# Kernel tuning notes

Hardware: AMD Instinct MI355X
Metric: run time of the kernel (lower is better)

The kernel has to match this reference:

```python
import jax, jax.numpy as jnp
import numpy as np
from jax import lax

B, L, F = 32, 2048, 76   # batch, seq_len, feat_dim
H = 128                  # conv hidden channels
D = 128                  # prototype dim (last 1x1 conv)
P = 128                  # number of prototypes
CLASS_SIZE = 2


def setup_inputs() -> dict:
    key = jax.random.key(0)
    ks = jax.random.split(key, 8)
    w = lambda k, shape: jax.random.normal(k, shape, jnp.float32) * 0.05
    return {
        "x": jax.random.normal(ks[0], (B, L, F), jnp.float32),
        "W1": w(ks[1], (H, F, 5)), "b1": jnp.zeros((H,), jnp.float32),
        "W2": w(ks[2], (H, H, 5)), "b2": jnp.zeros((H,), jnp.float32),
        "W3": w(ks[3], (H, H, 5)), "b3": jnp.zeros((H,), jnp.float32),
        "Wo1": w(ks[4], (D, H)), "bo1": jnp.zeros((D,), jnp.float32),
        "Wo2": w(ks[5], (D, D)), "bo2": jnp.zeros((D,), jnp.float32),
        "prototypes": jax.random.uniform(ks[6], (P, D), jnp.float32),
        "protop_classes": jnp.concatenate([jnp.zeros(P // 2, jnp.int32), jnp.ones(P // 2, jnp.int32)]),
    }


def _conv1d_same(h, W, b):
    # h: (B, C, L), W: (O, C, K=5), symmetric padding 2 == torch padding=k//2
    y = lax.conv_general_dilated(h, W, window_strides=(1,), padding=[(2, 2)],
                                 dimension_numbers=("NCW", "OIW", "NCW"))
    return y + b[None, :, None]


def _maxpool2(h):
    return lax.reduce_window(h, -jnp.inf, lax.max, (1, 1, 2), (1, 1, 2), "VALID")


def reference(x, W1, b1, W2, b2, W3, b3, Wo1, bo1, Wo2, bo2, prototypes, protop_classes):
    h = jnp.transpose(x, (0, 2, 1))  # (B, F, L)
    for W, b in ((W1, b1), (W2, b2), (W3, b3)):
        h = _maxpool2(jax.nn.relu(_conv1d_same(h, W, b)))
    # 1x1 convs as channel matmuls
    h = jax.nn.relu(jnp.einsum("bcl,oc->bol", h, Wo1) + bo1[None, :, None])
    h = jax.nn.relu(jnp.einsum("bcl,oc->bol", h, Wo2) + bo2[None, :, None])
    f = jnp.transpose(h, (0, 2, 1))  # (B, Lp=256, D)
    # l2_conv via ||a-b||^2 = ||a||^2 - 2 a.b + ||b||^2 (same math, GEMM form)
    d2 = (jnp.sum(f * f, axis=-1, keepdims=True)
          - 2.0 * jnp.einsum("bld,pd->blp", f, prototypes)
          + jnp.sum(prototypes * prototypes, axis=-1))  # (B, Lp, P)
    dis = jnp.sqrt(jnp.maximum(d2, 1e-12))
    min_dis = jnp.min(dis, axis=1)  # (B, P): min over patches
    # dis2sim, 'log' activation
    sim = jnp.log((min_dis + 1.0) / (min_dis + 1e-4))
    # init_weights: last_layer.weight[i,j] = 1 if protop_classes[j]==i else -0.5
    lw = jnp.where(protop_classes[None, :] == jnp.arange(CLASS_SIZE)[:, None], 1.0, -0.5)
    out = jax.nn.sigmoid(sim @ lw.T)  # (B, CLASS_SIZE)
    return out, min_dis
```

## Files before the change

kernel.cpp:

```cpp
#include <hip/hip_runtime.h>
#include <cmath>


typedef __attribute__((ext_vector_type(8))) short short8;
typedef __attribute__((ext_vector_type(4))) float f32x4;

__device__ __forceinline__ unsigned short f2bf(float v) {
    union { float f; unsigned u; } x; x.f = v;
    unsigned r = x.u + 0x7fffu + ((x.u >> 16) & 1u);
    return (unsigned short)(r >> 16);
}
__device__ __forceinline__ float bf2f(unsigned short b) {
    union { unsigned u; float f; } x; x.u = ((unsigned)b) << 16;
    return x.f;
}

__device__ void pack_conv_w(int t, int total, const float* __restrict__ W, int C,
                            unsigned short* __restrict__ dst)
{
    if (t >= total) return;
    int lane = t & 63, rest = t >> 6;
    int mf = rest & 7; rest >>= 3;
    int kk = rest % 5, cc = rest / 5;
    int m = mf * 16 + (lane & 15);
    int cb = cc * 32 + (lane >> 4) * 8;
    unsigned short v[8];
#pragma unroll
    for (int j = 0; j < 8; ++j) {
        int c = cb + j;
        v[j] = (c < C) ? f2bf(W[((size_t)m * C + c) * 5 + kk]) : (unsigned short)0;
    }
    *(uint4*)&dst[(size_t)t * 8] = *(uint4*)v;
}

__device__ void pack_mat(int t, const float* __restrict__ M, unsigned short* __restrict__ dst)
{
    if (t >= 2048) return;
    int lane = t & 63, mf = (t >> 6) & 7, cc = t >> 9;
    int m = mf * 16 + (lane & 15);
    int c0 = cc * 32 + (lane >> 4) * 8;
    unsigned short v[8];
#pragma unroll
    for (int j = 0; j < 8; ++j) v[j] = f2bf(M[(size_t)m * 128 + c0 + j]);
    *(uint4*)&dst[(size_t)t * 8] = *(uint4*)v;
}

__global__ __launch_bounds__(256)
void prep_weights_kernel(const float* __restrict__ W1, const float* __restrict__ W2,
                         const float* __restrict__ W3, const float* __restrict__ Wo1,
                         const float* __restrict__ Wo2, const float* __restrict__ protos,
                         unsigned short* A1, unsigned short* A2, unsigned short* A3,
                         unsigned short* AW1, unsigned short* AW2, unsigned short* AP,
                         float* pn, unsigned* pm_bits)
{
    int t = blockIdx.x * 256 + threadIdx.x;
    switch (blockIdx.y) {
    case 0: pack_conv_w(t, 7680,  W1, 76,  A1); break;
    case 1: pack_conv_w(t, 10240, W2, 128, A2); break;
    case 2: pack_conv_w(t, 10240, W3, 128, A3); break;
    case 3: pack_mat(t, Wo1, AW1); break;
    case 4: pack_mat(t, Wo2, AW2); break;
    case 5: pack_mat(t, protos, AP); break;
    case 6:
        if (t < 128) {
            float s = 0.f;
            for (int d = 0; d < 128; ++d) {
                float v = bf2f(f2bf(protos[(size_t)t * 128 + d]));
                s = fmaf(v, v, s);
            }
            pn[t] = s;
        }
        break;
    case 7:
        if (t < 4096) pm_bits[t] = 0x7F800000u;
        break;
    }
}

template <int NJ, int NCC, int STRIDE, int ROWOFF, int ROWMAX>
__device__ __forceinline__ void conv_k(const unsigned short* __restrict__ Af,
                                       const unsigned short* __restrict__ sIn,
                                       int nbase, int mf0, int lane,
                                       f32x4 (&acc)[2][NJ])
{
    const int lc = lane & 15;
    const int lk = (lane >> 4) * 8;
#pragma unroll
    for (int i = 0; i < 2; ++i)
#pragma unroll
        for (int j = 0; j < NJ; ++j) acc[i][j] = (f32x4){0.f, 0.f, 0.f, 0.f};

    for (int cc = 0; cc < NCC; ++cc) {
#pragma unroll
        for (int kk = 0; kk < 5; ++kk) {
            const int step = cc * 5 + kk;
            short8 a[2];
#pragma unroll
            for (int i = 0; i < 2; ++i)
                a[i] = *(const short8*)&Af[(((size_t)step * 8 + mf0 + i) * 64 + lane) * 8];
            short8 bb[NJ];
#pragma unroll
            for (int j = 0; j < NJ; ++j) {
                int row = nbase + j * 16 + lc + kk + ROWOFF;
                if (ROWMAX >= 0) row = min(max(row, 0), ROWMAX);
                bb[j] = *(const short8*)&sIn[row * STRIDE + cc * 32 + lk];
            }
#pragma unroll
            for (int j = 0; j < NJ; ++j)
#pragma unroll
                for (int i = 0; i < 2; ++i)
                    acc[i][j] = __builtin_amdgcn_mfma_f32_16x16x32_bf16(a[i], bb[j], acc[i][j], 0, 0, 0);
        }
    }
}

__device__ __forceinline__ void gemm_head(const unsigned short* __restrict__ Af,
                                          const unsigned short* __restrict__ s_f,
                                          int nbase, int mf0, int lane,
                                          f32x4 (&acc)[2])
{
    const int lc = lane & 15;
    const int lk = (lane >> 4) * 8;
    acc[0] = (f32x4){0.f, 0.f, 0.f, 0.f};
    acc[1] = (f32x4){0.f, 0.f, 0.f, 0.f};
#pragma unroll
    for (int cc = 0; cc < 4; ++cc) {
        short8 a[2];
#pragma unroll
        for (int i = 0; i < 2; ++i)
            a[i] = *(const short8*)&Af[(((size_t)cc * 8 + mf0 + i) * 64 + lane) * 8];
        short8 bb = *(const short8*)&s_f[(nbase + lc) * 136 + cc * 32 + lk];
#pragma unroll
        for (int i = 0; i < 2; ++i)
            acc[i] = __builtin_amdgcn_mfma_f32_16x16x32_bf16(a[i], bb, acc[i], 0, 0, 0);
    }
}

__global__ __launch_bounds__(512, 2)
void mega_kernel(const float* __restrict__ x,
                 const unsigned short* __restrict__ A1, const float* __restrict__ b1,
                 const unsigned short* __restrict__ A2, const float* __restrict__ b2,
                 const unsigned short* __restrict__ A3, const float* __restrict__ b3,
                 const unsigned short* __restrict__ AW1, const float* __restrict__ bo1,
                 const unsigned short* __restrict__ AW2, const float* __restrict__ bo2,
                 const unsigned short* __restrict__ AP,  const float* __restrict__ pn,
                 unsigned* __restrict__ pm_bits)
{
    __shared__ __align__(16) unsigned short s_x[324 * 104];
    __shared__ __align__(16) unsigned short s_h1[140 * 136];
    __shared__ float s_cb[768];
    __shared__ float s_part[128];
    __shared__ float s_fn[32];
    unsigned short* s_h2 = s_x;
    unsigned short* s_f  = s_x + 9248;

    const int tid  = threadIdx.x;
    const int q    = blockIdx.x;
    const int b    = blockIdx.y;
    const int lane = tid & 63;
    const int wid  = tid >> 6;
    const int mf0  = (wid & 3) * 2;
    const int ng   = wid >> 2;
    const int lc   = lane & 15;
    const int lq   = (lane >> 4) * 4;

    for (int i = tid; i < 768; i += 512) {
        const float* src = (i < 128) ? b1 : (i < 256) ? b2 : (i < 384) ? b3
                         : (i < 512) ? bo1 : (i < 640) ? bo2 : pn;
        s_cb[i] = src[i & 127];
    }

    const int xbase = 256 * q - 18;
    for (int idx = tid; idx < 324 * 24; idx += 512) {
        int pos = idx / 24, c0 = (idx % 24) * 4;
        int l = xbase + pos;
        unsigned short v[4] = {0, 0, 0, 0};
        if (c0 < 76 && l >= 0 && l < 2048) {
            float4 xv = *(const float4*)&x[((size_t)b * 2048 + l) * 76 + c0];
            v[0] = f2bf(xv.x); v[1] = f2bf(xv.y); v[2] = f2bf(xv.z); v[3] = f2bf(xv.w);
        }
        *(uint2*)&s_x[pos * 104 + c0] = *(uint2*)v;
    }
    __syncthreads();

    {
        f32x4 acc[2][10];
        conv_k<10, 3, 104, 0, -1>(A1, s_x, ng * 160, mf0, lane, acc);

#pragma unroll
        for (int i = 0; i < 2; ++i) {
            const int ch0 = (mf0 + i) * 16 + lq;
#pragma unroll
            for (int j = 0; j < 10; ++j) {
                const int nl = ng * 160 + j * 16 + lc;
                unsigned short pk[4];
#pragma unroll
                for (int r = 0; r < 4; ++r) {
                    float v = fmaxf(acc[i][j][r] + s_cb[ch0 + r], 0.f);
                    float o = __shfl_xor(v, 1);
                    pk[r] = f2bf(fmaxf(v, o));
                }
                if ((lc & 1) == 0) {
                    int jh = (nl >> 1) - 2;
                    int jg = 128 * q - 6 + jh;
                    if (jh >= 0 && jh < 140) {
                        uint2 val = (jg >= 0 && jg < 1024) ? *(uint2*)pk : make_uint2(0u, 0u);
                        *(uint2*)&s_h1[jh * 136 + ch0] = val;
                    }
                }
            }
        }
    }
    __syncthreads();

    {
        f32x4 acc[2][6];
        conv_k<6, 4, 136, -4, 139>(A2, s_h1, ng * 96, mf0, lane, acc);

#pragma unroll
        for (int i = 0; i < 2; ++i) {
            const int ch0 = (mf0 + i) * 16 + lq;
#pragma unroll
            for (int j = 0; j < 6; ++j) {
                const int nl = ng * 96 + j * 16 + lc;
                unsigned short pk[4];
#pragma unroll
                for (int r = 0; r < 4; ++r) {
                    float v = fmaxf(acc[i][j][r] + s_cb[128 + ch0 + r], 0.f);
                    float o = __shfl_xor(v, 1);
                    pk[r] = f2bf(fmaxf(v, o));
                }
                if ((lc & 1) == 0) {
                    int jh = (nl >> 1) - 2;
                    int jg = 64 * q - 2 + jh;
                    if (jh >= 0 && jh < 68) {
                        uint2 val = (jg >= 0 && jg < 512) ? *(uint2*)pk : make_uint2(0u, 0u);
                        *(uint2*)&s_h2[jh * 136 + ch0] = val;
                    }
                }
            }
        }
    }
    __syncthreads();

    {
        f32x4 acc[2][2];
        conv_k<2, 4, 136, 0, -1>(A3, s_h2, ng * 32, mf0, lane, acc);

#pragma unroll
        for (int i = 0; i < 2; ++i) {
            const int ch0 = (mf0 + i) * 16 + lq;
#pragma unroll
            for (int j = 0; j < 2; ++j) {
                const int nl = ng * 32 + j * 16 + lc;
                unsigned short pk[4];
#pragma unroll
                for (int r = 0; r < 4; ++r) {
                    float v = fmaxf(acc[i][j][r] + s_cb[256 + ch0 + r], 0.f);
                    float o = __shfl_xor(v, 1);
                    pk[r] = f2bf(fmaxf(v, o));
                }
                if ((lc & 1) == 0)
                    *(uint2*)&s_f[(nl >> 1) * 136 + ch0] = *(uint2*)pk;
            }
        }
    }
    __syncthreads();

    f32x4 hacc[2];

    gemm_head(AW1, s_f, ng * 16, mf0, lane, hacc);
    __syncthreads();
#pragma unroll
    for (int i = 0; i < 2; ++i) {
        const int ch0 = (mf0 + i) * 16 + lq;
        unsigned short pk[4];
#pragma unroll
        for (int r = 0; r < 4; ++r)
            pk[r] = f2bf(fmaxf(hacc[i][r] + s_cb[384 + ch0 + r], 0.f));
        *(uint2*)&s_f[(ng * 16 + lc) * 136 + ch0] = *(uint2*)pk;
    }
    __syncthreads();

    gemm_head(AW2, s_f, ng * 16, mf0, lane, hacc);
    __syncthreads();
#pragma unroll
    for (int i = 0; i < 2; ++i) {
        const int ch0 = (mf0 + i) * 16 + lq;
        unsigned short pk[4];
#pragma unroll
        for (int r = 0; r < 4; ++r)
            pk[r] = f2bf(fmaxf(hacc[i][r] + s_cb[512 + ch0 + r], 0.f));
        *(uint2*)&s_f[(ng * 16 + lc) * 136 + ch0] = *(uint2*)pk;
    }
    __syncthreads();

    if (tid < 128) {
        int n = tid >> 2, part = tid & 3;
        float s = 0.f;
        for (int c = part * 32; c < part * 32 + 32; ++c) {
            float v = bf2f(s_f[n * 136 + c]);
            s = fmaf(v, v, s);
        }
        s_part[part * 32 + n] = s;
    }
    __syncthreads();
    if (tid < 32)
        s_fn[tid] = s_part[tid] + s_part[32 + tid] + s_part[64 + tid] + s_part[96 + tid];
    __syncthreads();

    gemm_head(AP, s_f, ng * 16, mf0, lane, hacc);
#pragma unroll
    for (int i = 0; i < 2; ++i) {
#pragma unroll
        for (int r = 0; r < 4; ++r) {
            const int p = (mf0 + i) * 16 + lq + r;
            const int n = ng * 16 + lc;
            float d2 = s_fn[n] + s_cb[640 + p] - 2.f * hacc[i][r];
            float m = sqrtf(fmaxf(d2, 1e-12f));
#pragma unroll
            for (int s = 1; s < 16; s <<= 1)
                m = fminf(m, __shfl_xor(m, s));
            if (lc == 0)
                atomicMin(&pm_bits[(size_t)b * 128 + p], __float_as_uint(m));
        }
    }
}

__global__ __launch_bounds__(128)
void finalize_kernel(const float* __restrict__ pm,
                     const int* __restrict__ classes,
                     float* __restrict__ out)
{
    __shared__ float r0[128], r1[128];
    const int b = blockIdx.x, p = threadIdx.x;
    float m = pm[(size_t)b * 128 + p];
    out[64 + b * 128 + p] = m;

    float sim = logf((m + 1.0f) / (m + 1e-4f));
    int cls = classes[p];
    r0[p] = (cls == 0) ? sim : -0.5f * sim;
    r1[p] = (cls == 1) ? sim : -0.5f * sim;
    __syncthreads();
    for (int s = 64; s > 0; s >>= 1) {
        if (p < s) { r0[p] += r0[p + s]; r1[p] += r1[p + s]; }
        __syncthreads();
    }
    if (p == 0) {
        out[b * 2 + 0] = 1.f / (1.f + expf(-r0[0]));
        out[b * 2 + 1] = 1.f / (1.f + expf(-r1[0]));
    }
}

extern "C" void kernel_launch(void* const* d_in, const int* in_sizes, int n_in,
                              void* d_out, int out_size, void* d_ws, size_t ws_size,
                              hipStream_t stream)
{
    (void)in_sizes; (void)n_in; (void)out_size; (void)ws_size;
    const float* x    = (const float*)d_in[0];
    const float* W1   = (const float*)d_in[1];
    const float* b1   = (const float*)d_in[2];
    const float* W2   = (const float*)d_in[3];
    const float* b2   = (const float*)d_in[4];
    const float* W3   = (const float*)d_in[5];
    const float* b3   = (const float*)d_in[6];
    const float* Wo1  = (const float*)d_in[7];
    const float* bo1  = (const float*)d_in[8];
    const float* Wo2  = (const float*)d_in[9];
    const float* bo2  = (const float*)d_in[10];
    const float* prot = (const float*)d_in[11];
    const int*   cls  = (const int*)d_in[12];
    float* out = (float*)d_out;

    char* ws = (char*)d_ws;
    unsigned short* A1  = (unsigned short*)(ws);
    unsigned short* A2  = (unsigned short*)(ws + 122880);
    unsigned short* A3  = (unsigned short*)(ws + 286720);
    unsigned short* AW1 = (unsigned short*)(ws + 450560);
    unsigned short* AW2 = (unsigned short*)(ws + 483328);
    unsigned short* AP  = (unsigned short*)(ws + 516096);
    float*          pn  = (float*)(ws + 548864);
    unsigned*       pm  = (unsigned*)(ws + 549376);

    prep_weights_kernel<<<dim3(40, 8), 256, 0, stream>>>(W1, W2, W3, Wo1, Wo2, prot,
                                                         A1, A2, A3, AW1, AW2, AP, pn, pm);
    mega_kernel<<<dim3(8, 32), 512, 0, stream>>>(x, A1, b1, A2, b2, A3, b3,
                                                 AW1, bo1, AW2, bo2, AP, pn, pm);
    finalize_kernel<<<32, 128, 0, stream>>>((const float*)pm, cls, out);
}
```

Measured before the change: 130.4 us.

## Halve sequence tile per block and widen per-wave channel tiles

Each block now covers 128 input positions instead of 256, using 256 threads and a 16x32 grid, which doubles the block count to better fill the CUs. Each wave now computes 4 channel fragments instead of 2, reusing each loaded B fragment across more MFMAs. The halo overhead per block grows relatively (196 rows loaded for 128 outputs), so there is more redundant conv work at the tile edges. Register pressure per wave also rises from the larger accumulator arrays.

Measured after the change: 130.2 us. No clear change (-0.1%).

```diff
diff --git a/kernel.cpp b/kernel.cpp
--- a/kernel.cpp
+++ b/kernel.cpp
@@ -77,16 +77,16 @@
     }
 }
 
-template <int NJ, int NCC, int STRIDE, int ROWOFF, int ROWMAX>
+template <int NJ, int NCC, int STRIDE, int ROWMAX>
 __device__ __forceinline__ void conv_k(const unsigned short* __restrict__ Af,
                                        const unsigned short* __restrict__ sIn,
                                        int nbase, int mf0, int lane,
-                                       f32x4 (&acc)[2][NJ])
+                                       f32x4 (&acc)[4][NJ])
 {
     const int lc = lane & 15;
     const int lk = (lane >> 4) * 8;
 #pragma unroll
-    for (int i = 0; i < 2; ++i)
+    for (int i = 0; i < 4; ++i)
 #pragma unroll
         for (int j = 0; j < NJ; ++j) acc[i][j] = (f32x4){0.f, 0.f, 0.f, 0.f};
 
@@ -94,21 +94,21 @@
 #pragma unroll
         for (int kk = 0; kk < 5; ++kk) {
             const int step = cc * 5 + kk;
-            short8 a[2];
-#pragma unroll
-            for (int i = 0; i < 2; ++i)
+            short8 a[4];
+#pragma unroll
+            for (int i = 0; i < 4; ++i)
                 a[i] = *(const short8*)&Af[(((size_t)step * 8 + mf0 + i) * 64 + lane) * 8];
             short8 bb[NJ];
 #pragma unroll
             for (int j = 0; j < NJ; ++j) {
-                int row = nbase + j * 16 + lc + kk + ROWOFF;
-                if (ROWMAX >= 0) row = min(max(row, 0), ROWMAX);
+                int row = nbase + j * 16 + lc + kk;
+                if (ROWMAX >= 0) row = min(row, ROWMAX);
                 bb[j] = *(const short8*)&sIn[row * STRIDE + cc * 32 + lk];
             }
 #pragma unroll
             for (int j = 0; j < NJ; ++j)
 #pragma unroll
-                for (int i = 0; i < 2; ++i)
+                for (int i = 0; i < 4; ++i)
                     acc[i][j] = __builtin_amdgcn_mfma_f32_16x16x32_bf16(a[i], bb[j], acc[i][j], 0, 0, 0);
         }
     }
@@ -116,8 +116,7 @@
 
 __device__ __forceinline__ void gemm_head(const unsigned short* __restrict__ Af,
                                           const unsigned short* __restrict__ s_f,
-                                          int nbase, int mf0, int lane,
-                                          f32x4 (&acc)[2])
+                                          int mf0h, int lane, f32x4 (&acc)[2])
 {
     const int lc = lane & 15;
     const int lk = (lane >> 4) * 8;
@@ -128,15 +127,15 @@
         short8 a[2];
 #pragma unroll
         for (int i = 0; i < 2; ++i)
-            a[i] = *(const short8*)&Af[(((size_t)cc * 8 + mf0 + i) * 64 + lane) * 8];
-        short8 bb = *(const short8*)&s_f[(nbase + lc) * 136 + cc * 32 + lk];
+            a[i] = *(const short8*)&Af[(((size_t)cc * 8 + mf0h + i) * 64 + lane) * 8];
+        short8 bb = *(const short8*)&s_f[lc * 136 + cc * 32 + lk];
 #pragma unroll
         for (int i = 0; i < 2; ++i)
             acc[i] = __builtin_amdgcn_mfma_f32_16x16x32_bf16(a[i], bb, acc[i], 0, 0, 0);
     }
 }
 
-__global__ __launch_bounds__(512, 2)
+__global__ __launch_bounds__(256, 2)
 void mega_kernel(const float* __restrict__ x,
                  const unsigned short* __restrict__ A1, const float* __restrict__ b1,
                  const unsigned short* __restrict__ A2, const float* __restrict__ b2,
@@ -146,32 +145,33 @@
                  const unsigned short* __restrict__ AP,  const float* __restrict__ pn,
                  unsigned* __restrict__ pm_bits)
 {
-    __shared__ __align__(16) unsigned short s_x[324 * 104];
-    __shared__ __align__(16) unsigned short s_h1[140 * 136];
+    __shared__ __align__(16) unsigned short s_x[196 * 104];
+    __shared__ __align__(16) unsigned short s_h1[84 * 136];
     __shared__ float s_cb[768];
-    __shared__ float s_part[128];
-    __shared__ float s_fn[32];
+    __shared__ float s_part[64];
+    __shared__ float s_fn[16];
     unsigned short* s_h2 = s_x;
-    unsigned short* s_f  = s_x + 9248;
+    unsigned short* s_f  = s_x + 5440;
 
     const int tid  = threadIdx.x;
-    const int q    = blockIdx.x;
+    const int u    = blockIdx.x;
     const int b    = blockIdx.y;
     const int lane = tid & 63;
     const int wid  = tid >> 6;
-    const int mf0  = (wid & 3) * 2;
-    const int ng   = wid >> 2;
+    const int mg   = wid & 1;
+    const int ng   = wid >> 1;
+    const int mf0  = mg * 4;
     const int lc   = lane & 15;
     const int lq   = (lane >> 4) * 4;
 
-    for (int i = tid; i < 768; i += 512) {
+    for (int i = tid; i < 768; i += 256) {
         const float* src = (i < 128) ? b1 : (i < 256) ? b2 : (i < 384) ? b3
                          : (i < 512) ? bo1 : (i < 640) ? bo2 : pn;
         s_cb[i] = src[i & 127];
     }
 
-    const int xbase = 256 * q - 18;
-    for (int idx = tid; idx < 324 * 24; idx += 512) {
+    const int xbase = 128 * u - 14;
+    for (int idx = tid; idx < 196 * 24; idx += 256) {
         int pos = idx / 24, c0 = (idx % 24) * 4;
         int l = xbase + pos;
         unsigned short v[4] = {0, 0, 0, 0};
@@ -184,15 +184,15 @@
     __syncthreads();
 
     {
-        f32x4 acc[2][10];
-        conv_k<10, 3, 104, 0, -1>(A1, s_x, ng * 160, mf0, lane, acc);
-
-#pragma unroll
-        for (int i = 0; i < 2; ++i) {
+        f32x4 acc[4][6];
+        conv_k<6, 3, 104, -1>(A1, s_x, ng * 96, mf0, lane, acc);
+
+#pragma unroll
+        for (int i = 0; i < 4; ++i) {
             const int ch0 = (mf0 + i) * 16 + lq;
 #pragma unroll
-            for (int j = 0; j < 10; ++j) {
-                const int nl = ng * 160 + j * 16 + lc;
+            for (int j = 0; j < 6; ++j) {
+                const int nl = ng * 96 + j * 16 + lc;
                 unsigned short pk[4];
 #pragma unroll
                 for (int r = 0; r < 4; ++r) {
@@ -201,11 +201,11 @@
                     pk[r] = f2bf(fmaxf(v, o));
                 }
                 if ((lc & 1) == 0) {
-                    int jh = (nl >> 1) - 2;
-                    int jg = 128 * q - 6 + jh;
-                    if (jh >= 0 && jh < 140) {
+                    int rr = nl >> 1;
+                    int jg = 64 * u - 6 + rr;
+                    if (rr < 84) {
                         uint2 val = (jg >= 0 && jg < 1024) ? *(uint2*)pk : make_uint2(0u, 0u);
-                        *(uint2*)&s_h1[jh * 136 + ch0] = val;
+                        *(uint2*)&s_h1[rr * 136 + ch0] = val;
                     }
                 }
             }
@@ -214,15 +214,15 @@
     __syncthreads();
 
     {
-        f32x4 acc[2][6];
-        conv_k<6, 4, 136, -4, 139>(A2, s_h1, ng * 96, mf0, lane, acc);
-
-#pragma unroll
-        for (int i = 0; i < 2; ++i) {
+        f32x4 acc[4][3];
+        conv_k<3, 4, 136, 83>(A2, s_h1, ng * 48, mf0, lane, acc);
+
+#pragma unroll
+        for (int i = 0; i < 4; ++i) {
             const int ch0 = (mf0 + i) * 16 + lq;
 #pragma unroll
-            for (int j = 0; j < 6; ++j) {
-                const int nl = ng * 96 + j * 16 + lc;
+            for (int j = 0; j < 3; ++j) {
+                const int nl = ng * 48 + j * 16 + lc;
                 unsigned short pk[4];
 #pragma unroll
                 for (int r = 0; r < 4; ++r) {
@@ -231,11 +231,11 @@
                     pk[r] = f2bf(fmaxf(v, o));
                 }
                 if ((lc & 1) == 0) {
-                    int jh = (nl >> 1) - 2;
-                    int jg = 64 * q - 2 + jh;
-                    if (jh >= 0 && jh < 68) {
+                    int rr = nl >> 1;
+                    int jg = 32 * u - 2 + rr;
+                    if (rr < 40) {
                         uint2 val = (jg >= 0 && jg < 512) ? *(uint2*)pk : make_uint2(0u, 0u);
-                        *(uint2*)&s_h2[jh * 136 + ch0] = val;
+                        *(uint2*)&s_h2[rr * 136 + ch0] = val;
                     }
                 }
             }
@@ -244,79 +244,77 @@
     __syncthreads();
 
     {
-        f32x4 acc[2][2];
-        conv_k<2, 4, 136, 0, -1>(A3, s_h2, ng * 32, mf0, lane, acc);
-
-#pragma unroll
-        for (int i = 0; i < 2; ++i) {
+        f32x4 acc[4][1];
+        conv_k<1, 4, 136, -1>(A3, s_h2, ng * 16, mf0, lane, acc);
+
+#pragma unroll
+        for (int i = 0; i < 4; ++i) {
             const int ch0 = (mf0 + i) * 16 + lq;
-#pragma unroll
-            for (int j = 0; j < 2; ++j) {
-                const int nl = ng * 32 + j * 16 + lc;
-                unsigned short pk[4];
-#pragma unroll
-                for (int r = 0; r < 4; ++r) {
-                    float v = fmaxf(acc[i][j][r] + s_cb[256 + ch0 + r], 0.f);
-                    float o = __shfl_xor(v, 1);
-                    pk[r] = f2bf(fmaxf(v, o));
-                }
-                if ((lc & 1) == 0)
-                    *(uint2*)&s_f[(nl >> 1) * 136 + ch0] = *(uint2*)pk;
-            }
-        }
-    }
-    __syncthreads();
-
+            const int nl = ng * 16 + lc;
+            unsigned short pk[4];
+#pragma unroll
+            for (int r = 0; r < 4; ++r) {
+                float v = fmaxf(acc[i][0][r] + s_cb[256 + ch0 + r], 0.f);
+                float o = __shfl_xor(v, 1);
+                pk[r] = f2bf(fmaxf(v, o));
+            }
+            if ((lc & 1) == 0)
+                *(uint2*)&s_f[(nl >> 1) * 136 + ch0] = *(uint2*)pk;
+        }
+    }
+    __syncthreads();
+
+    const int mf0h = wid * 2;
     f32x4 hacc[2];
 
-    gemm_head(AW1, s_f, ng * 16, mf0, lane, hacc);
+    gemm_head(AW1, s_f, mf0h, lane, hacc);
     __syncthreads();
 #pragma unroll
     for (int i = 0; i < 2; ++i) {
-        const int ch0 = (mf0 + i) * 16 + lq;
+        const int ch0 = (mf0h + i) * 16 + lq;
         unsigned short pk[4];
 #pragma unroll
         for (int r = 0; r < 4; ++r)
             pk[r] = f2bf(fmaxf(hacc[i][r] + s_cb[384 + ch0 + r], 0.f));
-        *(uint2*)&s_f[(ng * 16 + lc) * 136 + ch0] = *(uint2*)pk;
-    }
-    __syncthreads();
-
-    gemm_head(AW2, s_f, ng * 16, mf0, lane, hacc);
+        *(uint2*)&s_f[lc * 136 + ch0] = *(uint2*)pk;
+    }
+    __syncthreads();
+
+    gemm_head(AW2, s_f, mf0h, lane, hacc);
     __syncthreads();
 #pragma unroll
     for (int i = 0; i < 2; ++i) {
-        const int ch0 = (mf0 + i) * 16 + lq;
+        const int ch0 = (mf0h + i) * 16 + lq;
         unsigned short pk[4];
 #pragma unroll
         for (int r = 0; r < 4; ++r)
             pk[r] = f2bf(fmaxf(hacc[i][r] + s_cb[512 + ch0 + r], 0.f));
-        *(uint2*)&s_f[(ng * 16 + lc) * 136 + ch0] = *(uint2*)pk;
-    }
-    __syncthreads();
-
-    if (tid < 128) {
+        *(uint2*)&s_f[lc * 136 + ch0] = *(uint2*)pk;
+    }
+    __syncthreads();
+
+    if (tid < 64) {
         int n = tid >> 2, part = tid & 3;
         float s = 0.f;
         for (int c = part * 32; c < part * 32 + 32; ++c) {
             float v = bf2f(s_f[n * 136 + c]);
             s = fmaf(v, v, s);
         }
-        s_part[part * 32 + n] = s;
-    }
-    __syncthreads();
-    if (tid < 32)
-        s_fn[tid] = s_part[tid] + s_part[32 + tid] + s_part[64 + tid] + s_part[96 + tid];
-    __syncthreads();
-
-    gemm_head(AP, s_f, ng * 16, mf0, lane, hacc);
+        s_part[part * 16 + n] = s;
+    }
+    __syncthreads();
+    if (tid < 16)
+        s_fn[tid] = s_part[tid] + s_part[16 + tid] + s_part[32 + tid] + s_part[48 + tid];
+    __syncthreads();
+
+    gemm_head(AP, s_f, mf0h, lane, hacc);
+
 #pragma unroll
     for (int i = 0; i < 2; ++i) {
 #pragma unroll
         for (int r = 0; r < 4; ++r) {
-            const int p = (mf0 + i) * 16 + lq + r;
-            const int n = ng * 16 + lc;
-            float d2 = s_fn[n] + s_cb[640 + p] - 2.f * hacc[i][r];
+            const int p = (mf0h + i) * 16 + lq + r;
+            float d2 = s_fn[lc] + s_cb[640 + p] - 2.f * hacc[i][r];
             float m = sqrtf(fmaxf(d2, 1e-12f));
 #pragma unroll
             for (int s = 1; s < 16; s <<= 1)
@@ -384,7 +382,7 @@
 
     prep_weights_kernel<<<dim3(40, 8), 256, 0, stream>>>(W1, W2, W3, Wo1, Wo2, prot,
                                                          A1, A2, A3, AW1, AW2, AP, pn, pm);
-    mega_kernel<<<dim3(8, 32), 512, 0, stream>>>(x, A1, b1, A2, b2, A3, b3,
-                                                 AW1, bo1, AW2, bo2, AP, pn, pm);
+    mega_kernel<<<dim3(16, 32), 256, 0, stream>>>(x, A1, b1, A2, b2, A3, b3,
+                                                  AW1, bo1, AW2, bo2, AP, pn, pm);
     finalize_kernel<<<32, 128, 0, stream>>>((const float*)pm, cls, out);
 }
```
